# Kernel optimization log

Measured on AMD Instinct MI355X. Metric: run time of the kernel, lower is better.

## Reference

```python
import jax, jax.numpy as jnp
from jax import lax
import numpy as np

D = 8        # domain_num
L = 12       # label_num
C = 9        # attr_num
W = 128      # window_size
B = 4096
EPS = 1e-5


def setup_inputs() -> dict:
    key = jax.random.key(0)
    ks = jax.random.split(key, 12)
    s = 0.05
    return {
        "x": jax.random.normal(ks[0], (B, C, 1, W), dtype=jnp.float32),
        "weights": jax.random.uniform(ks[1], (B, D), dtype=jnp.float32),
        # per-domain stacked parameters (leading dim D)
        "gamma": jnp.ones((D, C), dtype=jnp.float32),
        "beta": jnp.zeros((D, C), dtype=jnp.float32),
        "w1": jax.random.normal(ks[2], (D, 32, C, 9), dtype=jnp.float32) * s,
        "b1": jax.random.normal(ks[3], (D, 32), dtype=jnp.float32) * s,
        "w2": jax.random.normal(ks[4], (D, 64, 32, 9), dtype=jnp.float32) * s,
        "b2": jax.random.normal(ks[5], (D, 64), dtype=jnp.float32) * s,
        "fcw": jax.random.normal(ks[6], (D, L, 64 * 26), dtype=jnp.float32) * s,
        "fcb": jax.random.normal(ks[7], (D, L), dtype=jnp.float32) * s,
    }


def _maxpool2(h):
    # MaxPool along width, kernel 2 stride 2 (height is 1 and already squeezed)
    b, c, w = h.shape
    return h.reshape(b, c, w // 2, 2).max(axis=-1)


def _branch(x3, gamma, beta, w1, b1, w2, b2, fcw, fcb):
    # x3: [B, C, W]. BatchNorm2d in training mode: batch stats over (N, H, W).
    mean = x3.mean(axis=(0, 2), keepdims=True)
    var = x3.var(axis=(0, 2), keepdims=True)
    xn = (x3 - mean) * lax.rsqrt(var + EPS) * gamma[None, :, None] + beta[None, :, None]
    dn = ('NCH', 'OIH', 'NCH')
    h = lax.conv_general_dilated(xn, w1, (1,), 'VALID', dimension_numbers=dn)
    h = _maxpool2(jax.nn.relu(h + b1[None, :, None]))          # [B,32,60]
    h = lax.conv_general_dilated(h, w2, (1,), 'VALID', dimension_numbers=dn)
    h = _maxpool2(jax.nn.relu(h + b2[None, :, None]))          # [B,64,26]
    flat = h.reshape(h.shape[0], 64 * 26)
    return jax.nn.relu(flat @ fcw.T + fcb)                      # [B,L]


def reference(x, weights, gamma, beta, w1, b1, w2, b2, fcw, fcb):
    x3 = x[:, :, 0, :]  # squeeze height=1 -> [B,C,W]
    per_domain = jax.vmap(_branch, in_axes=(None, 0, 0, 0, 0, 0, 0, 0, 0))(
        x3, gamma, beta, w1, b1, w2, b2, fcw, fcb)              # [D,B,L]
    # vectorized form of the nested python-loop weighted sum over domains
    return jnp.einsum('bd,dbl->bl', weights, per_domain)        # [B,L]
```

## Files before the change

kernel.cpp:

```cpp
#include <hip/hip_runtime.h>
#include <hip/hip_bf16.h>

#define D 8
#define L 12
#define C 9
#define W 128
#define B 4096
#define EPS 1e-5f

typedef __attribute__((ext_vector_type(8))) short v8s;
typedef __attribute__((ext_vector_type(4))) float v4f;

#define OFF_STATS 0
#define OFF_B1E   1152
#define OFF_W1T   1408
#define OFF_W2T   21888
#define OFF_FCWP  95616

__device__ inline unsigned short f2bf(float f) {
    unsigned u = __builtin_bit_cast(unsigned, f);
    u += 0x7FFFu + ((u >> 16) & 1u);
    return (unsigned short)(u >> 16);
}
__device__ inline unsigned pk2(float a, float b) {
    float2 f2; f2.x = a; f2.y = b;
    __hip_bfloat162 h = __float22bfloat162_rn(f2);
    unsigned u; __builtin_memcpy(&u, &h, 4);
    return u;
}

__global__ void stats_repack_kernel(const float* __restrict__ x,
                                    const float* __restrict__ w2,
                                    const float* __restrict__ fcw,
                                    float* __restrict__ ws) {
    const int t = threadIdx.x;
    __shared__ float redS[8];
    if (blockIdx.x < 576) {
        const int c = blockIdx.x % 9;
        const int slice = blockIdx.x / 9;
        const int w4 = t & 31, br = t >> 5;
        const float4* x4 = (const float4*)x;
        float s = 0.f, s2 = 0.f;
        for (int b = slice * 8 + br; b < B; b += 64 * 8) {
            float4 v = x4[(size_t)b * 288 + c * 32 + w4];
            s  += v.x + v.y + v.z + v.w;
            s2 += v.x * v.x + v.y * v.y + v.z * v.z + v.w * v.w;
        }
        for (int off = 32; off >= 1; off >>= 1) {
            s  += __shfl_down(s, off);
            s2 += __shfl_down(s2, off);
        }
        if ((t & 63) == 0) { redS[(t >> 6) * 2] = s; redS[(t >> 6) * 2 + 1] = s2; }
        __syncthreads();
        if (t == 0) {
            ws[OFF_STATS + slice * 18 + c]     = redS[0] + redS[2] + redS[4] + redS[6];
            ws[OFF_STATS + slice * 18 + 9 + c] = redS[1] + redS[3] + redS[5] + redS[7];
        }
    } else {
        const int i0 = blockIdx.x - 576;
        const int d = i0 / 5, part = i0 % 5;
        short* w2t  = (short*)(ws + OFF_W2T);
        short* fcwp = (short*)(ws + OFF_FCWP);
        if (part < 2) {
            for (int i = part * 256 + t; i < 64 * 9 * 32; i += 512) {
                int o = i / 288, r = i % 288, tap = r / 32, ic = r & 31;
                w2t[(size_t)d * 18432 + i] =
                    (short)f2bf(w2[(((size_t)(d * 64 + o)) * 32 + ic) * 9 + tap]);
            }
        } else {
            for (int i = (part - 2) * 256 + t; i < 12 * 1664; i += 768) {
                int l = i / 1664, k = i % 1664, p = k >> 6, o = k & 63;
                fcwp[((size_t)d * 12) * 1664 + i] =
                    (short)f2bf(fcw[((size_t)(d * 12 + l)) * 1664 + o * 26 + p]);
            }
        }
    }
}

__global__ void fold1_kernel(const float* __restrict__ w1, const float* __restrict__ b1,
                             const float* __restrict__ gamma, const float* __restrict__ beta,
                             float* __restrict__ ws) {
    const int d = blockIdx.x, t = threadIdx.x;
    __shared__ float g[9], bt[9];
    if (t < 64) {
        for (int c = 0; c < 9; c++) {
            float s  = ws[OFF_STATS + t * 18 + c];
            float s2 = ws[OFF_STATS + t * 18 + 9 + c];
            for (int off = 32; off >= 1; off >>= 1) {
                s  += __shfl_down(s, off);
                s2 += __shfl_down(s2, off);
            }
            if (t == 0) {
                const float N = (float)B * (float)W;
                float m  = s / N;
                float vv = s2 / N - m * m;
                float inv = rsqrtf(vv + EPS);
                float gg = gamma[d * 9 + c] * inv;
                g[c] = gg; bt[c] = beta[d * 9 + c] - gg * m;
            }
        }
    }
    __syncthreads();
    const int o = t >> 3, sub = t & 7;
    short* w1t = (short*)(ws + OFF_W1T);
    short* dst = w1t + (size_t)d * 5120 + o * 160;
    const float* src = w1 + ((size_t)(d * 32 + o)) * 81;
    float bias_part = 0.f;
    for (int tap = sub; tap < 10; tap += 8) {
        for (int c = 0; c < 16; c++) {
            float v = 0.f;
            if (tap < 9 && c < 9) {
                float wv = src[c * 9 + tap];
                v = wv * g[c];
                bias_part += wv * bt[c];
            }
            dst[tap * 16 + c] = (short)f2bf(v);
        }
    }
    bias_part += __shfl_xor(bias_part, 1);
    bias_part += __shfl_xor(bias_part, 2);
    bias_part += __shfl_xor(bias_part, 4);
    if (sub == 0) ws[OFF_B1E + d * 32 + o] = b1[d * 32 + o] + bias_part;
}

__global__ __launch_bounds__(256, 4)
void branch_kernel(const float* __restrict__ x,
                   const float* __restrict__ b2g,
                   const float* __restrict__ fcb,
                   const float* __restrict__ wts,
                   const float* __restrict__ ws,
                   float* __restrict__ out) {
    const int t = threadIdx.x;
    const int lane = t & 63;
    const int wv = __builtin_amdgcn_readfirstlane(t >> 6);
    const int d = blockIdx.y;
    const int b0 = blockIdx.x * 4;
    const short* w1t  = (const short*)(ws + OFF_W1T) + (size_t)d * 5120;
    const short* w2t  = (const short*)(ws + OFF_W2T) + (size_t)d * 18432;
    const short* fcwp = (const short*)(ws + OFF_FCWP) + (size_t)d * 12 * 1664;
    const float* b1e  = ws + OFF_B1E + d * 32;

    __shared__ __align__(16) short ldsB[9216];
    __shared__ __align__(16) short ldsA[9344];
    short* xb  = ldsB;
    short* h1t = ldsA;
    short* h2p = ldsB;
    float* red = (float*)ldsA;

    const int n = lane & 15, quad = lane >> 4;

    {
        const float* xrow = x + (size_t)(b0 + wv) * 1152;
        #pragma unroll
        for (int rep = 0; rep < 2; rep++) {
            const int w = lane + rep * 64;
            float v[9];
            #pragma unroll
            for (int c = 0; c < 9; c++) v[c] = xrow[c * 128 + w];
            uint4 lo, hi;
            lo.x = pk2(v[0], v[1]); lo.y = pk2(v[2], v[3]);
            lo.z = pk2(v[4], v[5]); lo.w = pk2(v[6], v[7]);
            hi.x = (unsigned)(unsigned short)f2bf(v[8]); hi.y = 0; hi.z = 0; hi.w = 0;
            *(uint4*)&xb[((wv * 2 + 0) * 144 + w) * 8] = lo;
            *(uint4*)&xb[((wv * 2 + 1) * 144 + w) * 8] = hi;
        }
        if (lane < 16) {
            uint4 z; z.x = z.y = z.z = z.w = 0;
            *(uint4*)&xb[((wv * 2 + 0) * 144 + 128 + lane) * 8] = z;
            *(uint4*)&xb[((wv * 2 + 1) * 144 + 128 + lane) * 8] = z;
        }
    }
    __syncthreads();

    {
        const int qh = quad >> 1, ql = quad & 1;
        v4f acc[8][2];
        #pragma unroll
        for (int mt = 0; mt < 8; mt++)
            #pragma unroll
            for (int nt = 0; nt < 2; nt++) { v4f z = {0.f,0.f,0.f,0.f}; acc[mt][nt] = z; }
        const float bias0 = b1e[n], bias1 = b1e[16 + n];
        #pragma unroll
        for (int s = 0; s < 5; s++) {
            v8s Bw0 = *(const v8s*)&w1t[n * 160 + (2 * s + qh) * 16 + ql * 8];
            v8s Bw1 = *(const v8s*)&w1t[(16 + n) * 160 + (2 * s + qh) * 16 + ql * 8];
            #pragma unroll
            for (int mt = 0; mt < 8; mt++) {
                const int row = mt * 16 + n + 2 * s + qh;
                v8s Af = *(const v8s*)&xb[((wv * 2 + ql) * 144 + row) * 8];
                acc[mt][0] = __builtin_amdgcn_mfma_f32_16x16x32_bf16(Af, Bw0, acc[mt][0], 0, 0, 0);
                acc[mt][1] = __builtin_amdgcn_mfma_f32_16x16x32_bf16(Af, Bw1, acc[mt][1], 0, 0, 0);
            }
        }
        #pragma unroll
        for (int mt = 0; mt < 8; mt++) {
            const int p = mt * 8 + quad * 2;
            #pragma unroll
            for (int nt = 0; nt < 2; nt++) {
                const float bb = nt ? bias1 : bias0;
                float h0  = fmaxf(fmaxf(acc[mt][nt][0], acc[mt][nt][1]) + bb, 0.f);
                float h1v = fmaxf(fmaxf(acc[mt][nt][2], acc[mt][nt][3]) + bb, 0.f);
                unsigned pr = pk2(h0, h1v);
                const int plane = wv * 4 + nt * 2 + (n >> 3);
                const int col = n & 7;
                if (p < 60)     h1t[(plane * 73 + p) * 8 + col]     = (short)(pr & 0xFFFFu);
                if (p + 1 < 60) h1t[(plane * 73 + p + 1) * 8 + col] = (short)(pr >> 16);
            }
        }
    }
    __syncthreads();

    {
        v4f acc[4][4];
        #pragma unroll
        for (int mt = 0; mt < 4; mt++)
            #pragma unroll
            for (int nt = 0; nt < 4; nt++) { v4f z = {0.f,0.f,0.f,0.f}; acc[mt][nt] = z; }
        float biasv[4];
        #pragma unroll
        for (int nt = 0; nt < 4; nt++) biasv[nt] = b2g[d * 64 + nt * 16 + n];
        for (int tap = 0; tap < 9; tap++) {
            v8s Bw[4];
            #pragma unroll
            for (int nt = 0; nt < 4; nt++)
                Bw[nt] = *(const v8s*)&w2t[(nt * 16 + n) * 288 + tap * 32 + quad * 8];
            #pragma unroll
            for (int mt = 0; mt < 4; mt++) {
                const int row = mt * 16 + n + tap;
                v8s Af = *(const v8s*)&h1t[((wv * 4 + quad) * 73 + row) * 8];
                #pragma unroll
                for (int nt = 0; nt < 4; nt++)
                    acc[mt][nt] = __builtin_amdgcn_mfma_f32_16x16x32_bf16(Af, Bw[nt], acc[mt][nt], 0, 0, 0);
            }
        }
        #pragma unroll
        for (int mt = 0; mt < 4; mt++) {
            const int p = mt * 8 + quad * 2;
            #pragma unroll
            for (int nt = 0; nt < 4; nt++) {
                float h0  = fmaxf(fmaxf(acc[mt][nt][0], acc[mt][nt][1]) + biasv[nt], 0.f);
                float h1v = fmaxf(fmaxf(acc[mt][nt][2], acc[mt][nt][3]) + biasv[nt], 0.f);
                unsigned pr = pk2(h0, h1v);
                const int oc = nt * 16 + n;
                if (p < 26) {
                    const int gs = (oc >> 3) ^ (p & 7);
                    h2p[wv * 1672 + p * 64 + gs * 8 + (oc & 7)] = (short)(pr & 0xFFFFu);
                }
                if (p + 1 < 26) {
                    const int gs = (oc >> 3) ^ ((p + 1) & 7);
                    h2p[wv * 1672 + (p + 1) * 64 + gs * 8 + (oc & 7)] = (short)(pr >> 16);
                }
            }
        }
    }
    __syncthreads();

    {
        const int lrow = (n < 12) ? n : 0;
        v4f acc = {0.f, 0.f, 0.f, 0.f};
        for (int ks = wv; ks < 52; ks += 4) {
            const int p = ks >> 1;
            const int gs = ((ks & 1) * 4 + quad) ^ (p & 7);
            v8s A  = *(const v8s*)&fcwp[lrow * 1664 + ks * 32 + quad * 8];
            v8s Bf = *(const v8s*)&h2p[(n & 3) * 1672 + p * 64 + gs * 8];
            acc = __builtin_amdgcn_mfma_f32_16x16x32_bf16(A, Bf, acc, 0, 0, 0);
        }
        *(float4*)&red[(wv * 64 + lane) * 4] = *(float4*)&acc;
    }
    __syncthreads();
    if (t < 64) {
        float sum[4] = {0.f, 0.f, 0.f, 0.f};
        #pragma unroll
        for (int w = 0; w < 4; w++) {
            float4 v = *(const float4*)&red[(w * 64 + lane) * 4];
            sum[0] += v.x; sum[1] += v.y; sum[2] += v.z; sum[3] += v.w;
        }
        if (n < 4) {
            const float wgt = wts[(size_t)(b0 + n) * 8 + d];
            #pragma unroll
            for (int r = 0; r < 4; r++) {
                const int l = quad * 4 + r;
                if (l < 12) {
                    float v = fmaxf(sum[r] + fcb[d * 12 + l], 0.f);
                    atomicAdd(&out[(size_t)(b0 + n) * 12 + l], wgt * v);
                }
            }
        }
    }
}

extern "C" void kernel_launch(void* const* d_in, const int* in_sizes, int n_in,
                              void* d_out, int out_size, void* d_ws, size_t ws_size,
                              hipStream_t stream) {
    const float* x       = (const float*)d_in[0];
    const float* weights = (const float*)d_in[1];
    const float* gamma   = (const float*)d_in[2];
    const float* beta    = (const float*)d_in[3];
    const float* w1      = (const float*)d_in[4];
    const float* b1      = (const float*)d_in[5];
    const float* w2      = (const float*)d_in[6];
    const float* b2      = (const float*)d_in[7];
    const float* fcw     = (const float*)d_in[8];
    const float* fcb     = (const float*)d_in[9];
    float* ws  = (float*)d_ws;
    float* out = (float*)d_out;

    (void)hipMemsetAsync(out, 0, (size_t)out_size * sizeof(float), stream);
    stats_repack_kernel<<<dim3(616), 256, 0, stream>>>(x, w2, fcw, ws);
    fold1_kernel<<<dim3(D), 256, 0, stream>>>(w1, b1, gamma, beta, ws);
    branch_kernel<<<dim3(B / 4, D), 256, 0, stream>>>(x, b2, fcb, weights, ws, out);
}
```

Measured before the change: 236.0 us.

## Use per-wave LDS regions, drop block barriers, split accumulators for occupancy

Each wave now works in its own 2304-short LDS slice, reused in place for input, conv1 output, conv2 output and the reduction scratch. This shrinks shared memory from two buffers to one and removes the two block-wide barriers between the early stages. Conv1 and conv2 now compute their accumulators in two halves and keep the packed results in registers before writing them back, which lowers peak register use. Launch bounds rise from 4 to 6 blocks per SIMD to raise occupancy. The cost is more repeated weight-fragment loads per half and a tighter register budget, which could cause spills.

Result: slower. 668.7 us (+183.3%).

```diff
diff --git a/kernel.cpp b/kernel.cpp
--- a/kernel.cpp
+++ b/kernel.cpp
@@ -123,7 +123,7 @@
     if (sub == 0) ws[OFF_B1E + d * 32 + o] = b1[d * 32 + o] + bias_part;
 }
 
-__global__ __launch_bounds__(256, 4)
+__global__ __launch_bounds__(256, 6)
 void branch_kernel(const float* __restrict__ x,
                    const float* __restrict__ b2g,
                    const float* __restrict__ fcb,
@@ -132,7 +132,7 @@
                    float* __restrict__ out) {
     const int t = threadIdx.x;
     const int lane = t & 63;
-    const int wv = __builtin_amdgcn_readfirstlane(t >> 6);
+    const int wv = t >> 6;
     const int d = blockIdx.y;
     const int b0 = blockIdx.x * 4;
     const short* w1t  = (const short*)(ws + OFF_W1T) + (size_t)d * 5120;
@@ -140,12 +140,8 @@
     const short* fcwp = (const short*)(ws + OFF_FCWP) + (size_t)d * 12 * 1664;
     const float* b1e  = ws + OFF_B1E + d * 32;
 
-    __shared__ __align__(16) short ldsB[9216];
-    __shared__ __align__(16) short ldsA[9344];
-    short* xb  = ldsB;
-    short* h1t = ldsA;
-    short* h2p = ldsB;
-    float* red = (float*)ldsA;
+    __shared__ __align__(16) short lds[9216];
+    short* myr = &lds[wv * 2304];
 
     const int n = lane & 15, quad = lane >> 4;
 
@@ -161,94 +157,112 @@
             lo.x = pk2(v[0], v[1]); lo.y = pk2(v[2], v[3]);
             lo.z = pk2(v[4], v[5]); lo.w = pk2(v[6], v[7]);
             hi.x = (unsigned)(unsigned short)f2bf(v[8]); hi.y = 0; hi.z = 0; hi.w = 0;
-            *(uint4*)&xb[((wv * 2 + 0) * 144 + w) * 8] = lo;
-            *(uint4*)&xb[((wv * 2 + 1) * 144 + w) * 8] = hi;
+            *(uint4*)&myr[(0 * 144 + w) * 8] = lo;
+            *(uint4*)&myr[(1 * 144 + w) * 8] = hi;
         }
         if (lane < 16) {
             uint4 z; z.x = z.y = z.z = z.w = 0;
-            *(uint4*)&xb[((wv * 2 + 0) * 144 + 128 + lane) * 8] = z;
-            *(uint4*)&xb[((wv * 2 + 1) * 144 + 128 + lane) * 8] = z;
-        }
-    }
-    __syncthreads();
+            *(uint4*)&myr[(0 * 144 + 128 + lane) * 8] = z;
+            *(uint4*)&myr[(1 * 144 + 128 + lane) * 8] = z;
+        }
+    }
 
     {
         const int qh = quad >> 1, ql = quad & 1;
-        v4f acc[8][2];
-        #pragma unroll
-        for (int mt = 0; mt < 8; mt++)
-            #pragma unroll
-            for (int nt = 0; nt < 2; nt++) { v4f z = {0.f,0.f,0.f,0.f}; acc[mt][nt] = z; }
         const float bias0 = b1e[n], bias1 = b1e[16 + n];
-        #pragma unroll
-        for (int s = 0; s < 5; s++) {
-            v8s Bw0 = *(const v8s*)&w1t[n * 160 + (2 * s + qh) * 16 + ql * 8];
-            v8s Bw1 = *(const v8s*)&w1t[(16 + n) * 160 + (2 * s + qh) * 16 + ql * 8];
-            #pragma unroll
-            for (int mt = 0; mt < 8; mt++) {
-                const int row = mt * 16 + n + 2 * s + qh;
-                v8s Af = *(const v8s*)&xb[((wv * 2 + ql) * 144 + row) * 8];
-                acc[mt][0] = __builtin_amdgcn_mfma_f32_16x16x32_bf16(Af, Bw0, acc[mt][0], 0, 0, 0);
-                acc[mt][1] = __builtin_amdgcn_mfma_f32_16x16x32_bf16(Af, Bw1, acc[mt][1], 0, 0, 0);
-            }
+        unsigned held[16];
+        #pragma unroll
+        for (int half = 0; half < 2; half++) {
+            v4f acc[4][2];
+            #pragma unroll
+            for (int m = 0; m < 4; m++)
+                #pragma unroll
+                for (int nt = 0; nt < 2; nt++) { v4f z = {0.f,0.f,0.f,0.f}; acc[m][nt] = z; }
+            #pragma unroll
+            for (int s = 0; s < 5; s++) {
+                v8s Bw0 = *(const v8s*)&w1t[n * 160 + (2 * s + qh) * 16 + ql * 8];
+                v8s Bw1 = *(const v8s*)&w1t[(16 + n) * 160 + (2 * s + qh) * 16 + ql * 8];
+                #pragma unroll
+                for (int m = 0; m < 4; m++) {
+                    const int row = (half * 4 + m) * 16 + n + 2 * s + qh;
+                    v8s Af = *(const v8s*)&myr[(ql * 144 + row) * 8];
+                    acc[m][0] = __builtin_amdgcn_mfma_f32_16x16x32_bf16(Af, Bw0, acc[m][0], 0, 0, 0);
+                    acc[m][1] = __builtin_amdgcn_mfma_f32_16x16x32_bf16(Af, Bw1, acc[m][1], 0, 0, 0);
+                }
+            }
+            #pragma unroll
+            for (int m = 0; m < 4; m++)
+                #pragma unroll
+                for (int nt = 0; nt < 2; nt++) {
+                    const float bb = nt ? bias1 : bias0;
+                    float h0  = fmaxf(fmaxf(acc[m][nt][0], acc[m][nt][1]) + bb, 0.f);
+                    float h1v = fmaxf(fmaxf(acc[m][nt][2], acc[m][nt][3]) + bb, 0.f);
+                    held[(half * 4 + m) * 2 + nt] = pk2(h0, h1v);
+                }
         }
         #pragma unroll
         for (int mt = 0; mt < 8; mt++) {
             const int p = mt * 8 + quad * 2;
             #pragma unroll
             for (int nt = 0; nt < 2; nt++) {
-                const float bb = nt ? bias1 : bias0;
-                float h0  = fmaxf(fmaxf(acc[mt][nt][0], acc[mt][nt][1]) + bb, 0.f);
-                float h1v = fmaxf(fmaxf(acc[mt][nt][2], acc[mt][nt][3]) + bb, 0.f);
-                unsigned pr = pk2(h0, h1v);
-                const int plane = wv * 4 + nt * 2 + (n >> 3);
+                const unsigned pr = held[mt * 2 + nt];
+                const int plane = nt * 2 + (n >> 3);
                 const int col = n & 7;
-                if (p < 60)     h1t[(plane * 73 + p) * 8 + col]     = (short)(pr & 0xFFFFu);
-                if (p + 1 < 60) h1t[(plane * 73 + p + 1) * 8 + col] = (short)(pr >> 16);
-            }
-        }
-    }
-    __syncthreads();
+                if (p < 60)     myr[(plane * 72 + p) * 8 + col]     = (short)(pr & 0xFFFFu);
+                if (p + 1 < 60) myr[(plane * 72 + p + 1) * 8 + col] = (short)(pr >> 16);
+            }
+        }
+    }
 
     {
-        v4f acc[4][4];
-        #pragma unroll
-        for (int mt = 0; mt < 4; mt++)
-            #pragma unroll
-            for (int nt = 0; nt < 4; nt++) { v4f z = {0.f,0.f,0.f,0.f}; acc[mt][nt] = z; }
         float biasv[4];
         #pragma unroll
         for (int nt = 0; nt < 4; nt++) biasv[nt] = b2g[d * 64 + nt * 16 + n];
-        for (int tap = 0; tap < 9; tap++) {
-            v8s Bw[4];
-            #pragma unroll
-            for (int nt = 0; nt < 4; nt++)
-                Bw[nt] = *(const v8s*)&w2t[(nt * 16 + n) * 288 + tap * 32 + quad * 8];
-            #pragma unroll
-            for (int mt = 0; mt < 4; mt++) {
-                const int row = mt * 16 + n + tap;
-                v8s Af = *(const v8s*)&h1t[((wv * 4 + quad) * 73 + row) * 8];
+        unsigned held[16];
+        #pragma unroll
+        for (int half = 0; half < 2; half++) {
+            v4f acc[2][4];
+            #pragma unroll
+            for (int m = 0; m < 2; m++)
+                #pragma unroll
+                for (int nt = 0; nt < 4; nt++) { v4f z = {0.f,0.f,0.f,0.f}; acc[m][nt] = z; }
+            for (int tap = 0; tap < 9; tap++) {
+                v8s Bw[4];
                 #pragma unroll
                 for (int nt = 0; nt < 4; nt++)
-                    acc[mt][nt] = __builtin_amdgcn_mfma_f32_16x16x32_bf16(Af, Bw[nt], acc[mt][nt], 0, 0, 0);
-            }
+                    Bw[nt] = *(const v8s*)&w2t[(nt * 16 + n) * 288 + tap * 32 + quad * 8];
+                #pragma unroll
+                for (int m = 0; m < 2; m++) {
+                    const int row = (half * 2 + m) * 16 + n + tap;
+                    v8s Af = *(const v8s*)&myr[(quad * 72 + row) * 8];
+                    #pragma unroll
+                    for (int nt = 0; nt < 4; nt++)
+                        acc[m][nt] = __builtin_amdgcn_mfma_f32_16x16x32_bf16(Af, Bw[nt], acc[m][nt], 0, 0, 0);
+                }
+            }
+            #pragma unroll
+            for (int m = 0; m < 2; m++)
+                #pragma unroll
+                for (int nt = 0; nt < 4; nt++) {
+                    float h0  = fmaxf(fmaxf(acc[m][nt][0], acc[m][nt][1]) + biasv[nt], 0.f);
+                    float h1v = fmaxf(fmaxf(acc[m][nt][2], acc[m][nt][3]) + biasv[nt], 0.f);
+                    held[(half * 2 + m) * 4 + nt] = pk2(h0, h1v);
+                }
         }
         #pragma unroll
         for (int mt = 0; mt < 4; mt++) {
             const int p = mt * 8 + quad * 2;
             #pragma unroll
             for (int nt = 0; nt < 4; nt++) {
-                float h0  = fmaxf(fmaxf(acc[mt][nt][0], acc[mt][nt][1]) + biasv[nt], 0.f);
-                float h1v = fmaxf(fmaxf(acc[mt][nt][2], acc[mt][nt][3]) + biasv[nt], 0.f);
-                unsigned pr = pk2(h0, h1v);
+                const unsigned pr = held[mt * 4 + nt];
                 const int oc = nt * 16 + n;
                 if (p < 26) {
                     const int gs = (oc >> 3) ^ (p & 7);
-                    h2p[wv * 1672 + p * 64 + gs * 8 + (oc & 7)] = (short)(pr & 0xFFFFu);
+                    myr[p * 64 + gs * 8 + (oc & 7)] = (short)(pr & 0xFFFFu);
                 }
                 if (p + 1 < 26) {
                     const int gs = (oc >> 3) ^ ((p + 1) & 7);
-                    h2p[wv * 1672 + (p + 1) * 64 + gs * 8 + (oc & 7)] = (short)(pr >> 16);
+                    myr[(p + 1) * 64 + gs * 8 + (oc & 7)] = (short)(pr >> 16);
                 }
             }
         }
@@ -262,17 +276,19 @@
             const int p = ks >> 1;
             const int gs = ((ks & 1) * 4 + quad) ^ (p & 7);
             v8s A  = *(const v8s*)&fcwp[lrow * 1664 + ks * 32 + quad * 8];
-            v8s Bf = *(const v8s*)&h2p[(n & 3) * 1672 + p * 64 + gs * 8];
+            v8s Bf = *(const v8s*)&lds[(n & 3) * 2304 + p * 64 + gs * 8];
             acc = __builtin_amdgcn_mfma_f32_16x16x32_bf16(A, Bf, acc, 0, 0, 0);
         }
-        *(float4*)&red[(wv * 64 + lane) * 4] = *(float4*)&acc;
+        float* red = (float*)(myr + 1672);
+        *(float4*)&red[lane * 4] = *(float4*)&acc;
     }
     __syncthreads();
     if (t < 64) {
         float sum[4] = {0.f, 0.f, 0.f, 0.f};
         #pragma unroll
         for (int w = 0; w < 4; w++) {
-            float4 v = *(const float4*)&red[(w * 64 + lane) * 4];
+            const float* redw = (const float*)(&lds[w * 2304 + 1672]);
+            float4 v = *(const float4*)&redw[lane * 4];
             sum[0] += v.x; sum[1] += v.y; sum[2] += v.z; sum[3] += v.w;
         }
         if (n < 4) {
```
